# Performance work log

Measured on AMD Instinct MI355X. Metric: run time of the kernel, lower is better.

Reference implementation:

```python
import jax, jax.numpy as jnp
import numpy as np
import math

N_LEVELS = 4          # quadtree depth; leaves = 4**4 = 256
N_HEAD = 8
LN_EPS = 1e-5

def _tree_consts():
    # level d has 4**d nodes; offsets[d] = first node index of level d
    sizes = [4 ** d for d in range(N_LEVELS + 1)]
    offsets = np.concatenate([[0], np.cumsum(sizes)])
    n_nodes = int(offsets[-1])  # 341
    parent = np.full(n_nodes, -1, np.int64)
    for d in range(1, N_LEVELS + 1):
        idx = offsets[d] + np.arange(sizes[d])
        parent[idx] = offsets[d - 1] + np.arange(sizes[d]) // 4
    # chain[c, k] = k-th ancestor of c (k=0 -> self); padded by clamping at root
    chain = np.zeros((n_nodes, N_LEVELS + 1), np.int64)
    chain[:, 0] = np.arange(n_nodes)
    for k in range(1, N_LEVELS + 1):
        prev = chain[:, k - 1]
        chain[:, k] = np.where(parent[prev] >= 0, parent[prev], prev)
    nodes_at = [offsets[d] + np.arange(sizes[d]) for d in range(N_LEVELS + 1)]
    return chain, nodes_at, n_nodes

CHAIN, NODES_AT, N_NODES = _tree_consts()

def layernorm(x, g, b):
    m = jnp.mean(x, -1, keepdims=True)
    v = jnp.var(x, -1, keepdims=True)
    return (x - m) * jax.lax.rsqrt(v + LN_EPS) * g + b

def mhsa(x, w_qkv, b_qkv, w_proj, b_proj):
    B, N, E = x.shape
    hd = E // N_HEAD
    qkv = x @ w_qkv + b_qkv                       # (B, N, 3E)
    q, k, v = jnp.split(qkv, 3, axis=-1)
    sh = lambda t: t.reshape(B, N, N_HEAD, hd).transpose(0, 2, 1, 3)  # (B,H,N,hd)
    q, k, v = sh(q), sh(k), sh(v)
    att = jax.nn.softmax(jnp.einsum('bhqd,bhkd->bhqk', q, k) / math.sqrt(hd), axis=-1)
    o = jnp.einsum('bhqk,bhkd->bhqd', att, v).transpose(0, 2, 1, 3).reshape(B, N, E)
    return o @ w_proj + b_proj

def branch_mlp(x, M, b1, w2, b2):
    # Sparse equivalent of einsum('bni,bjmni->bmj', x, W1): W1[:, c, a, :]
    # is nonzero only for a in {c} U ancestors(c), with the weight matrix
    # depending only on (depth(c), depth(a)). Group nodes by depth and sum
    # over ancestor offsets k (depth(a) = d - k).
    B, N, E = x.shape
    h = jnp.zeros((B, N, 4 * E), x.dtype)
    for d in range(N_LEVELS + 1):
        nd = NODES_AT[d]                           # static numpy indices
        acc = jnp.zeros((B, nd.shape[0], 4 * E), x.dtype)
        for k in range(d + 1):
            src = CHAIN[nd, k]                     # ancestor at depth d-k
            acc = acc + jnp.einsum('bne,je->bnj', x[:, src, :], M[d, d - k])
        h = h.at[:, nd, :].set(acc)
    h = jax.nn.relu(h + b1[None, :, :])
    return h @ w2 + b2

def setup_inputs() -> dict:
    key = jax.random.key(0)
    ks = jax.random.split(key, 6)
    B, N, E = 64, N_NODES, 512
    s = 0.02
    return {
        'x': jax.random.normal(ks[0], (B, N, E), jnp.float32),
        'ln1_g': jnp.ones((E,), jnp.float32),
        'ln1_b': jnp.zeros((E,), jnp.float32),
        'w_qkv': jax.random.normal(ks[1], (E, 3 * E), jnp.float32) * s,
        'b_qkv': jnp.zeros((3 * E,), jnp.float32),
        'w_proj': jax.random.normal(ks[2], (E, E), jnp.float32) * s,
        'b_proj': jnp.zeros((E,), jnp.float32),
        'ln2_g': jnp.ones((E,), jnp.float32),
        'ln2_b': jnp.zeros((E,), jnp.float32),
        'mlp_M': jax.random.normal(ks[3], (N_LEVELS + 1, N_LEVELS + 1, 4 * E, E), jnp.float32) * s,
        'mlp_b1': jnp.zeros((N, 4 * E), jnp.float32),
        'w2': jax.random.normal(ks[4], (4 * E, E), jnp.float32) * s,
        'b2': jnp.zeros((E,), jnp.float32),
    }

def reference(x, ln1_g, ln1_b, w_qkv, b_qkv, w_proj, b_proj,
              ln2_g, ln2_b, mlp_M, mlp_b1, w2, b2):
    x = x + mhsa(layernorm(x, ln1_g, ln1_b), w_qkv, b_qkv, w_proj, b_proj)
    x = x + branch_mlp(layernorm(x, ln2_g, ln2_b), mlp_M, mlp_b1, w2, b2)
    return x
```

## Files before the change

### kernel.cpp

```cpp
#include <hip/hip_runtime.h>
#include <hip/hip_bf16.h>


typedef __attribute__((ext_vector_type(8))) __bf16 bf16x8;
typedef __attribute__((ext_vector_type(4))) float f32x4;
typedef __attribute__((ext_vector_type(4))) unsigned int u32x4;

#define GF_RELU    1
#define GF_OUTBF16 2

static __device__ __forceinline__ bf16x8 bzero8() {
    u32x4 z = {0u, 0u, 0u, 0u};
    return __builtin_bit_cast(bf16x8, z);
}

__global__ void transpose_bf16_kernel(const float* __restrict__ in,
                                      __hip_bfloat16* __restrict__ out,
                                      int K, int N, int log2K) {
    int idx = blockIdx.x * 256 + threadIdx.x;
    if (idx >= K * N) return;
    int n = idx >> log2K;
    int k = idx & (K - 1);
    out[idx] = __float2bfloat16(in[(size_t)k * N + n]);
}

__global__ void pack_wcat_kernel(const float* __restrict__ M,
                                 __hip_bfloat16* __restrict__ out) {
    int p = blockIdx.y;
    int s, d;
    if (p < 5)       { s = 0; d = p; }
    else if (p < 9)  { s = 1; d = p - 4; }
    else if (p < 12) { s = 2; d = p - 7; }
    else if (p < 14) { s = 3; d = p - 9; }
    else             { s = 4; d = 4; }
    const int base_lut[5] = {0, 5, 9, 12, 14};
    size_t idx = (size_t)blockIdx.x * 256 + threadIdx.x;
    const size_t MB = 2048ull * 512;
    out[(size_t)base_lut[s] * MB + (size_t)(d - s) * MB + idx] =
        __float2bfloat16(M[((size_t)d * 5 + s) * MB + idx]);
}

__global__ __launch_bounds__(256) void ln_kernel(const float* __restrict__ x,
                                                 const float* __restrict__ g,
                                                 const float* __restrict__ b,
                                                 __hip_bfloat16* __restrict__ out) {
    int tok = blockIdx.x;
    const float* xr = x + (size_t)tok * 512;
    int t = threadIdx.x;
    float v0 = xr[t], v1 = xr[t + 256];
    float s = v0 + v1;
    float s2 = v0 * v0 + v1 * v1;
    #pragma unroll
    for (int o = 32; o > 0; o >>= 1) {
        s  += __shfl_down(s, o);
        s2 += __shfl_down(s2, o);
    }
    __shared__ float ps[4], ps2[4];
    int w = t >> 6, lane = t & 63;
    if (lane == 0) { ps[w] = s; ps2[w] = s2; }
    __syncthreads();
    if (t == 0) {
        float ts = 0.f, ts2 = 0.f;
        #pragma unroll
        for (int i = 0; i < 4; i++) { ts += ps[i]; ts2 += ps2[i]; }
        ps[0] = ts * (1.f / 512.f);
        ps2[0] = ts2 * (1.f / 512.f);
    }
    __syncthreads();
    float m = ps[0];
    float var = ps2[0] - m * m;
    float r = rsqrtf(var + 1e-5f);
    out[(size_t)tok * 512 + t]       = __float2bfloat16((v0 - m) * r * g[t] + b[t]);
    out[(size_t)tok * 512 + t + 256] = __float2bfloat16((v1 - m) * r * g[t + 256] + b[t + 256]);
}

#define ATT_STR 72
__global__ __launch_bounds__(256) void attn_mfma_kernel(const __hip_bfloat16* __restrict__ qkv,
                                                        __hip_bfloat16* __restrict__ ctx) {
    __shared__ __bf16 kt_lds[64 * ATT_STR];
    __shared__ __bf16 vt_lds[64 * ATT_STR];
    __shared__ __bf16 pbuf[4 * 48 * ATT_STR];

    const int bh = blockIdx.x;
    const int half = blockIdx.y;
    const int b = bh >> 3, h = bh & 7;
    const int tid = threadIdx.x;
    const int w = tid >> 6, lane = tid & 63;
    const int q = lane >> 4, l16 = lane & 15;
    const int rowbase = half * 192 + w * 48;
    __bf16* pw = pbuf + w * 48 * ATT_STR;

    bf16x8 qf[3][2];
    #pragma unroll
    for (int mi = 0; mi < 3; mi++) {
        int row = rowbase + mi * 16 + l16;
        #pragma unroll
        for (int ks = 0; ks < 2; ks++) {
            if (row < 341)
                qf[mi][ks] = *(const bf16x8*)(qkv + (size_t)(b * 341 + row) * 1536 +
                                              h * 64 + ks * 32 + q * 8);
            else
                qf[mi][ks] = bzero8();
        }
    }

    f32x4 O[3][4];
    float mrun[3][4], lrun[3][4];
    #pragma unroll
    for (int mi = 0; mi < 3; mi++) {
        #pragma unroll
        for (int ni = 0; ni < 4; ni++) { f32x4 z = {0.f,0.f,0.f,0.f}; O[mi][ni] = z; }
        #pragma unroll
        for (int rr = 0; rr < 4; rr++) { mrun[mi][rr] = -1e30f; lrun[mi][rr] = 0.f; }
    }

    for (int kt6 = 0; kt6 < 6; kt6++) {
        const int kbase = kt6 * 64;
        __syncthreads();
        {
            int key = tid >> 2, kg = tid & 3;
            int gk = kbase + key;
            bf16x8 a0 = bzero8(), a1 = bzero8();
            if (gk < 341) {
                const __hip_bfloat16* src =
                    qkv + (size_t)(b * 341 + gk) * 1536 + 512 + h * 64 + kg * 16;
                a0 = *(const bf16x8*)src;
                a1 = *(const bf16x8*)(src + 8);
            }
            *(bf16x8*)(kt_lds + key * ATT_STR + kg * 16)     = a0;
            *(bf16x8*)(kt_lds + key * ATT_STR + kg * 16 + 8) = a1;
        }
        {
            int key = tid & 63, dg = tid >> 6;
            int gk = kbase + key;
            bf16x8 a0 = bzero8(), a1 = bzero8();
            if (gk < 341) {
                const __hip_bfloat16* src =
                    qkv + (size_t)(b * 341 + gk) * 1536 + 1024 + h * 64 + dg * 16;
                a0 = *(const bf16x8*)src;
                a1 = *(const bf16x8*)(src + 8);
            }
            #pragma unroll
            for (int j = 0; j < 8; j++) {
                vt_lds[(dg * 16 + j) * ATT_STR + key]     = a0[j];
                vt_lds[(dg * 16 + 8 + j) * ATT_STR + key] = a1[j];
            }
        }
        __syncthreads();

        f32x4 S[3][4];
        #pragma unroll
        for (int mi = 0; mi < 3; mi++)
            #pragma unroll
            for (int ni = 0; ni < 4; ni++) { f32x4 z = {0.f,0.f,0.f,0.f}; S[mi][ni] = z; }
        #pragma unroll
        for (int ks = 0; ks < 2; ks++) {
            bf16x8 bf_[4];
            #pragma unroll
            for (int ni = 0; ni < 4; ni++)
                bf_[ni] = *(const bf16x8*)(kt_lds + (ni * 16 + l16) * ATT_STR + ks * 32 + q * 8);
            #pragma unroll
            for (int mi = 0; mi < 3; mi++)
                #pragma unroll
                for (int ni = 0; ni < 4; ni++)
                    S[mi][ni] = __builtin_amdgcn_mfma_f32_16x16x32_bf16(qf[mi][ks], bf_[ni],
                                                                        S[mi][ni], 0, 0, 0);
        }

        float cmask[4];
        #pragma unroll
        for (int ni = 0; ni < 4; ni++)
            cmask[ni] = (kbase + ni * 16 + l16 < 341) ? 0.f : -1e30f;

        #pragma unroll
        for (int mi = 0; mi < 3; mi++) {
            #pragma unroll
            for (int rr = 0; rr < 4; rr++) {
                float rmax = -1e30f;
                #pragma unroll
                for (int ni = 0; ni < 4; ni++)
                    rmax = fmaxf(rmax, fmaf(S[mi][ni][rr], 0.125f, cmask[ni]));
                rmax = fmaxf(rmax, __shfl_xor(rmax, 1));
                rmax = fmaxf(rmax, __shfl_xor(rmax, 2));
                rmax = fmaxf(rmax, __shfl_xor(rmax, 4));
                rmax = fmaxf(rmax, __shfl_xor(rmax, 8));
                float mnew = fmaxf(mrun[mi][rr], rmax);
                float alpha = __expf(mrun[mi][rr] - mnew);
                mrun[mi][rr] = mnew;
                float psum = 0.f;
                #pragma unroll
                for (int ni = 0; ni < 4; ni++) {
                    float p = __expf(fmaf(S[mi][ni][rr], 0.125f, cmask[ni]) - mnew);
                    S[mi][ni][rr] = p;
                    psum += p;
                    O[mi][ni][rr] *= alpha;
                }
                psum += __shfl_xor(psum, 1);
                psum += __shfl_xor(psum, 2);
                psum += __shfl_xor(psum, 4);
                psum += __shfl_xor(psum, 8);
                lrun[mi][rr] = lrun[mi][rr] * alpha + psum;
            }
            #pragma unroll
            for (int ni = 0; ni < 4; ni++)
                #pragma unroll
                for (int rr = 0; rr < 4; rr++)
                    pw[(mi * 16 + q * 4 + rr) * ATT_STR + ni * 16 + l16] =
                        (__bf16)S[mi][ni][rr];
        }
        __syncthreads();

        #pragma unroll
        for (int ks = 0; ks < 2; ks++) {
            bf16x8 pf[3], vf[4];
            #pragma unroll
            for (int mi = 0; mi < 3; mi++)
                pf[mi] = *(const bf16x8*)(pw + (mi * 16 + l16) * ATT_STR + ks * 32 + q * 8);
            #pragma unroll
            for (int ni = 0; ni < 4; ni++)
                vf[ni] = *(const bf16x8*)(vt_lds + (ni * 16 + l16) * ATT_STR + ks * 32 + q * 8);
            #pragma unroll
            for (int mi = 0; mi < 3; mi++)
                #pragma unroll
                for (int ni = 0; ni < 4; ni++)
                    O[mi][ni] = __builtin_amdgcn_mfma_f32_16x16x32_bf16(pf[mi], vf[ni],
                                                                        O[mi][ni], 0, 0, 0);
        }
    }

    #pragma unroll
    for (int mi = 0; mi < 3; mi++) {
        #pragma unroll
        for (int rr = 0; rr < 4; rr++) {
            int row = rowbase + mi * 16 + q * 4 + rr;
            if (row >= 341) continue;
            float inv = 1.f / lrun[mi][rr];
            __hip_bfloat16* op = ctx + (size_t)(b * 341 + row) * 512 + h * 64;
            #pragma unroll
            for (int ni = 0; ni < 4; ni++)
                op[ni * 16 + l16] = __float2bfloat16(O[mi][ni][rr] * inv);
        }
    }
}

static __device__ __forceinline__ int xcd_remap(int bid, int nwg) {
    const int xcd = bid & 7, o = bid >> 3;
    const int qq = nwg >> 3, rr = nwg & 7;
    return (xcd < rr ? xcd * (qq + 1) : rr * (qq + 1) + (xcd - rr) * qq) + o;
}

template <bool GATHER>
static __device__ __forceinline__ void gemm128_body(
    __hip_bfloat16* As, __hip_bfloat16* Bs,
    const __hip_bfloat16* __restrict__ A, const __hip_bfloat16* __restrict__ Bt,
    const float* __restrict__ bias, const float* __restrict__ resid,
    float* __restrict__ Cf, __hip_bfloat16* __restrict__ Cb,
    int Mrows, int N, int K, int flags, int depth, int bm0, int bn0) {
    const int tid = threadIdx.x;
    const int r = tid >> 1;
    const int khalf = tid & 1;
    const int gr = bm0 + r;
    const int gn = bn0 + r;
    const int lane = tid & 63;
    const int w = tid >> 6;
    const int wm = (w >> 1) << 6;
    const int wn = (w & 1) << 6;
    const int q = lane >> 4;
    const int l16 = lane & 15;

    int wsl[4];
    #pragma unroll
    for (int j = 0; j < 4; j++)
        wsl[j] = ((((khalf << 2) | j) ^ (r & 7)) << 3);
    const int rs0 = ((q ^ (l16 & 7)) << 3);
    const int rs1 = (((4 + q) ^ (l16 & 7)) << 3);

    size_t abase;
    if (GATHER) {
        const int dsh = depth << 1;
        const int bmask = (1 << dsh) - 1;
        int b = gr >> dsh;
        int i = gr & bmask;
        int node = (0x55555555 & bmask) + i;
        abase = ((size_t)(b * 341 + node)) << 9;
    } else {
        abase = (size_t)gr * K;
    }

    f32x4 acc[4][4];
    #pragma unroll
    for (int i = 0; i < 4; i++)
        #pragma unroll
        for (int j = 0; j < 4; j++) {
            f32x4 z = {0.f, 0.f, 0.f, 0.f};
            acc[i][j] = z;
        }

    for (int k0 = 0; k0 < K; k0 += 64) {
        bf16x8 va[4], vb[4];
        if (gr < Mrows) {
            const bf16x8* p = (const bf16x8*)(A + abase + k0 + (khalf << 5));
            #pragma unroll
            for (int j = 0; j < 4; j++) va[j] = p[j];
        } else {
            #pragma unroll
            for (int j = 0; j < 4; j++) va[j] = bzero8();
        }
        {
            const bf16x8* p = (const bf16x8*)(Bt + (size_t)gn * K + k0 + (khalf << 5));
            #pragma unroll
            for (int j = 0; j < 4; j++) vb[j] = p[j];
        }
        __syncthreads();
        #pragma unroll
        for (int j = 0; j < 4; j++) {
            *(bf16x8*)(As + r * 64 + wsl[j]) = va[j];
            *(bf16x8*)(Bs + r * 64 + wsl[j]) = vb[j];
        }
        __syncthreads();
        bf16x8 af[4][2], bfr[4][2];
        #pragma unroll
        for (int mi = 0; mi < 4; mi++) {
            const __hip_bfloat16* rp = As + (wm + mi * 16 + l16) * 64;
            af[mi][0] = *(const bf16x8*)(rp + rs0);
            af[mi][1] = *(const bf16x8*)(rp + rs1);
        }
        #pragma unroll
        for (int ni = 0; ni < 4; ni++) {
            const __hip_bfloat16* rp = Bs + (wn + ni * 16 + l16) * 64;
            bfr[ni][0] = *(const bf16x8*)(rp + rs0);
            bfr[ni][1] = *(const bf16x8*)(rp + rs1);
        }
        #pragma unroll
        for (int ks = 0; ks < 2; ks++)
            #pragma unroll
            for (int mi = 0; mi < 4; mi++)
                #pragma unroll
                for (int ni = 0; ni < 4; ni++)
                    acc[mi][ni] = __builtin_amdgcn_mfma_f32_16x16x32_bf16(
                        af[mi][ks], bfr[ni][ks], acc[mi][ni], 0, 0, 0);
    }

    #pragma unroll
    for (int mi = 0; mi < 4; mi++) {
        #pragma unroll
        for (int rr = 0; rr < 4; rr++) {
            int grow = bm0 + wm + mi * 16 + q * 4 + rr;
            if (grow >= Mrows) continue;
            size_t obase = (size_t)grow * N;
            #pragma unroll
            for (int ni = 0; ni < 4; ni++) {
                int col = bn0 + wn + ni * 16 + l16;
                float v = acc[mi][ni][rr];
                if (bias) v += bias[col];
                if (resid) v += resid[obase + col];
                if (flags & GF_RELU) v = fmaxf(v, 0.f);
                if (flags & GF_OUTBF16)
                    Cb[obase + col] = __float2bfloat16(v);
                else
                    Cf[obase + col] = v;
            }
        }
    }
}

__global__ __launch_bounds__(256) void gemm128(
    const __hip_bfloat16* __restrict__ A, const __hip_bfloat16* __restrict__ Bt,
    const float* __restrict__ bias, const float* __restrict__ resid,
    float* __restrict__ Cf, __hip_bfloat16* __restrict__ Cb,
    int Mrows, int N, int K, int flags, int gridN) {
    __shared__ __hip_bfloat16 As[128 * 64];
    __shared__ __hip_bfloat16 Bs[128 * 64];
    const int lin = xcd_remap(blockIdx.x, gridDim.x);
    const int bx = lin / gridN;
    const int by = lin - bx * gridN;
    gemm128_body<false>(As, Bs, A, Bt, bias, resid, Cf, Cb,
                        Mrows, N, K, flags, 0, bx << 7, by << 7);
}

__global__ __launch_bounds__(256, 4) void gemm64(
    const __hip_bfloat16* __restrict__ A, const __hip_bfloat16* __restrict__ Bt,
    const float* __restrict__ bias, const float* __restrict__ resid,
    float* __restrict__ Cf, __hip_bfloat16* __restrict__ Cb,
    int Mrows, int N, int K, int flags, int gridN) {
    __shared__ __hip_bfloat16 As[64 * 64];
    __shared__ __hip_bfloat16 Bs[128 * 64];
    const int lin = xcd_remap(blockIdx.x, gridDim.x);
    const int bx = lin / gridN;
    const int by = lin - bx * gridN;
    const int bm0 = bx << 6, bn0 = by << 7;

    const int tid = threadIdx.x;
    const int ra = tid >> 2, kq = tid & 3;
    const int rb = tid >> 1, khalf = tid & 1;
    const int lane = tid & 63;
    const int w = tid >> 6;
    const int wn = w << 5;
    const int q = lane >> 4;
    const int l16 = lane & 15;

    const int gra = bm0 + ra;
    const int gnb = bn0 + rb;

    int wslA[2];
    #pragma unroll
    for (int j = 0; j < 2; j++)
        wslA[j] = ((((kq << 1) | j) ^ (ra & 7)) << 3);
    int wslB[4];
    #pragma unroll
    for (int j = 0; j < 4; j++)
        wslB[j] = ((((khalf << 2) | j) ^ (rb & 7)) << 3);
    const int rs0 = ((q ^ (l16 & 7)) << 3);
    const int rs1 = (((4 + q) ^ (l16 & 7)) << 3);

    const size_t abase = (size_t)gra * K;

    f32x4 acc[4][2];
    #pragma unroll
    for (int i = 0; i < 4; i++)
        #pragma unroll
        for (int j = 0; j < 2; j++) {
            f32x4 z = {0.f, 0.f, 0.f, 0.f};
            acc[i][j] = z;
        }

    for (int k0 = 0; k0 < K; k0 += 64) {
        bf16x8 va[2], vb[4];
        if (gra < Mrows) {
            const bf16x8* p = (const bf16x8*)(A + abase + k0 + (kq << 4));
            #pragma unroll
            for (int j = 0; j < 2; j++) va[j] = p[j];
        } else {
            #pragma unroll
            for (int j = 0; j < 2; j++) va[j] = bzero8();
        }
        {
            const bf16x8* p = (const bf16x8*)(Bt + (size_t)gnb * K + k0 + (khalf << 5));
            #pragma unroll
            for (int j = 0; j < 4; j++) vb[j] = p[j];
        }
        __syncthreads();
        #pragma unroll
        for (int j = 0; j < 2; j++)
            *(bf16x8*)(As + ra * 64 + wslA[j]) = va[j];
        #pragma unroll
        for (int j = 0; j < 4; j++)
            *(bf16x8*)(Bs + rb * 64 + wslB[j]) = vb[j];
        __syncthreads();
        bf16x8 af[4][2], bfr[2][2];
        #pragma unroll
        for (int mi = 0; mi < 4; mi++) {
            const __hip_bfloat16* rp = As + (mi * 16 + l16) * 64;
            af[mi][0] = *(const bf16x8*)(rp + rs0);
            af[mi][1] = *(const bf16x8*)(rp + rs1);
        }
        #pragma unroll
        for (int ni = 0; ni < 2; ni++) {
            const __hip_bfloat16* rp = Bs + (wn + ni * 16 + l16) * 64;
            bfr[ni][0] = *(const bf16x8*)(rp + rs0);
            bfr[ni][1] = *(const bf16x8*)(rp + rs1);
        }
        #pragma unroll
        for (int ks = 0; ks < 2; ks++)
            #pragma unroll
            for (int mi = 0; mi < 4; mi++)
                #pragma unroll
                for (int ni = 0; ni < 2; ni++)
                    acc[mi][ni] = __builtin_amdgcn_mfma_f32_16x16x32_bf16(
                        af[mi][ks], bfr[ni][ks], acc[mi][ni], 0, 0, 0);
    }

    #pragma unroll
    for (int mi = 0; mi < 4; mi++) {
        #pragma unroll
        for (int rr = 0; rr < 4; rr++) {
            int grow = bm0 + mi * 16 + q * 4 + rr;
            if (grow >= Mrows) continue;
            size_t obase = (size_t)grow * N;
            #pragma unroll
            for (int ni = 0; ni < 2; ni++) {
                int col = bn0 + wn + ni * 16 + l16;
                float v = acc[mi][ni][rr];
                if (bias) v += bias[col];
                if (resid) v += resid[obase + col];
                if (flags & GF_RELU) v = fmaxf(v, 0.f);
                if (flags & GF_OUTBF16)
                    Cb[obase + col] = __float2bfloat16(v);
                else
                    Cf[obase + col] = v;
            }
        }
    }
}

__global__ __launch_bounds__(256) void gemm_branch_fused(
    const __hip_bfloat16* __restrict__ xn, const __hip_bfloat16* __restrict__ wcat,
    __hip_bfloat16* __restrict__ Y) {
    __shared__ __hip_bfloat16 As[128 * 64];
    __shared__ __hip_bfloat16 Bs[128 * 64];
    const int lin = xcd_remap(blockIdx.x, gridDim.x);
    int s;
    if (lin < 80)        s = 0;
    else if (lin < 208)  s = 1;
    else if (lin < 592)  s = 2;
    else if (lin < 1616) s = 3;
    else                 s = 4;
    const int base_tab[5] = {0, 80, 208, 592, 1616};
    const int gn_tab[5]   = {80, 64, 48, 32, 16};
    const size_t yoff[5]  = {0, 655360, 2752512, 9043968, 25821184};
    const int wcat_off[5] = {0, 5, 9, 12, 14};
    const int loc = lin - base_tab[s];
    const int gn = gn_tab[s];
    const int bx = loc / gn;
    const int by = loc - bx * gn;
    const int Mrows = 64 << (s << 1);
    const int N = (5 - s) << 11;
    gemm128_body<true>(As, Bs, xn, wcat + (size_t)wcat_off[s] * (2048ull * 512),
                       nullptr, nullptr, nullptr, Y + yoff[s],
                       Mrows, N, 512, GF_OUTBF16, s, bx << 7, by << 7);
}

__global__ __launch_bounds__(256) void combine_kernel(const __hip_bfloat16* __restrict__ Y,
                                                      const float* __restrict__ b1,
                                                      __hip_bfloat16* __restrict__ h) {
    const size_t yoff[5] = {0, 655360, 2752512, 9043968, 25821184};
    int row = blockIdx.x;
    int b = row / 341;
    int node = row - b * 341;
    int d = (node >= 85) ? 4 : (node >= 21) ? 3 : (node >= 5) ? 2 : (node >= 1) ? 1 : 0;
    int i = node - (0x55555555 & ((1 << (d << 1)) - 1));
    int j = threadIdx.x << 3;

    float acc[8];
    const float* bp = b1 + (size_t)node * 2048 + j;
    f32x4 b0 = *(const f32x4*)bp;
    f32x4 b4 = *(const f32x4*)(bp + 4);
    #pragma unroll
    for (int u = 0; u < 4; u++) { acc[u] = b0[u]; acc[u + 4] = b4[u]; }

    #pragma unroll
    for (int s = 0; s < 5; s++) {
        if (s <= d) {
            int a = i >> ((d - s) << 1);
            int width = (5 - s) << 11;
            const bf16x8 v = *(const bf16x8*)(Y + yoff[s] +
                (size_t)((b << (s << 1)) + a) * width + ((d - s) << 11) + j);
            #pragma unroll
            for (int u = 0; u < 8; u++) acc[u] += (float)v[u];
        }
    }
    bf16x8 o;
    #pragma unroll
    for (int u = 0; u < 8; u++) o[u] = (__bf16)fmaxf(acc[u], 0.f);
    *(bf16x8*)(h + (size_t)row * 2048 + j) = o;
}

extern "C" void kernel_launch(void* const* d_in, const int* in_sizes, int n_in,
                              void* d_out, int out_size, void* d_ws, size_t ws_size,
                              hipStream_t stream) {
    const float* x      = (const float*)d_in[0];
    const float* ln1_g  = (const float*)d_in[1];
    const float* ln1_b  = (const float*)d_in[2];
    const float* w_qkv  = (const float*)d_in[3];
    const float* b_qkv  = (const float*)d_in[4];
    const float* w_proj = (const float*)d_in[5];
    const float* b_proj = (const float*)d_in[6];
    const float* ln2_g  = (const float*)d_in[7];
    const float* ln2_b  = (const float*)d_in[8];
    const float* mlp_M  = (const float*)d_in[9];
    const float* mlp_b1 = (const float*)d_in[10];
    const float* w2     = (const float*)d_in[11];
    const float* b2     = (const float*)d_in[12];
    float* out = (float*)d_out;

    const int M = 64 * 341;

    char* ws = (char*)d_ws;
    size_t off = 0;
    auto alloc = [&](size_t bytes) -> char* {
        char* p = ws + off;
        off += (bytes + 255) & ~(size_t)255;
        return p;
    };
    __hip_bfloat16* xn     = (__hip_bfloat16*)alloc((size_t)M * 512 * 2);
    __hip_bfloat16* wqkvT  = (__hip_bfloat16*)alloc(1536ull * 512 * 2);
    __hip_bfloat16* wprojT = (__hip_bfloat16*)alloc(512ull * 512 * 2);
    __hip_bfloat16* w2T    = (__hip_bfloat16*)alloc(512ull * 2048 * 2);
    __hip_bfloat16* wcat   = (__hip_bfloat16*)alloc(15ull * 2048 * 512 * 2);
    __hip_bfloat16* hbuf   = (__hip_bfloat16*)alloc((size_t)M * 2048 * 2);
    const size_t qkv_bytes = (size_t)M * 1536 * 2;
    const size_t y_bytes   = 59375616ull * 2;
    char* shared = alloc(y_bytes);
    __hip_bfloat16* qkv = (__hip_bfloat16*)shared;
    __hip_bfloat16* ctx = (__hip_bfloat16*)(shared + qkv_bytes);
    __hip_bfloat16* Y   = (__hip_bfloat16*)shared;
    if (off > ws_size) return;

    auto g128 = [&](const __hip_bfloat16* A, const __hip_bfloat16* Bt,
                    const float* bias, const float* resid, float* Cf,
                    __hip_bfloat16* Cb, int Mr, int N, int K, int flags) {
        int gm = (Mr + 127) >> 7, gn = N >> 7;
        gemm128<<<dim3(gm * gn), 256, 0, stream>>>(
            A, Bt, bias, resid, Cf, Cb, Mr, N, K, flags, gn);
    };
    auto g64 = [&](const __hip_bfloat16* A, const __hip_bfloat16* Bt,
                   const float* bias, const float* resid, float* Cf,
                   __hip_bfloat16* Cb, int Mr, int N, int K, int flags) {
        int gm = (Mr + 63) >> 6, gn = N >> 7;
        gemm64<<<dim3(gm * gn), 256, 0, stream>>>(
            A, Bt, bias, resid, Cf, Cb, Mr, N, K, flags, gn);
    };

    transpose_bf16_kernel<<<(512 * 1536 + 255) / 256, 256, 0, stream>>>(w_qkv, wqkvT, 512, 1536, 9);
    transpose_bf16_kernel<<<(512 * 512 + 255) / 256, 256, 0, stream>>>(w_proj, wprojT, 512, 512, 9);
    transpose_bf16_kernel<<<(2048 * 512 + 255) / 256, 256, 0, stream>>>(w2, w2T, 2048, 512, 11);
    pack_wcat_kernel<<<dim3(4096, 15), 256, 0, stream>>>(mlp_M, wcat);

    ln_kernel<<<M, 256, 0, stream>>>(x, ln1_g, ln1_b, xn);
    g128(xn, wqkvT, b_qkv, nullptr, nullptr, qkv, M, 1536, 512, GF_OUTBF16);
    attn_mfma_kernel<<<dim3(512, 2), 256, 0, stream>>>(qkv, ctx);
    g64(ctx, wprojT, b_proj, x, out, nullptr, M, 512, 512, 0);

    ln_kernel<<<M, 256, 0, stream>>>(out, ln2_g, ln2_b, xn);
    gemm_branch_fused<<<dim3(3664), 256, 0, stream>>>(xn, wcat, Y);
    combine_kernel<<<M, 256, 0, stream>>>(Y, mlp_b1, hbuf);
    g64(hbuf, w2T, b2, out, out, nullptr, M, 512, 2048, 0);
}
```

Baseline: 722.1 us.

## Split K across two wave groups in gemm64 with LDS reduction

```diff
diff --git a/kernel.cpp b/kernel.cpp
--- a/kernel.cpp
+++ b/kernel.cpp
@@ -378,42 +378,45 @@
                         Mrows, N, K, flags, 0, bx << 7, by << 7);
 }
 
-__global__ __launch_bounds__(256, 4) void gemm64(
+__global__ __launch_bounds__(512, 2) void gemm64k2(
     const __hip_bfloat16* __restrict__ A, const __hip_bfloat16* __restrict__ Bt,
     const float* __restrict__ bias, const float* __restrict__ resid,
     float* __restrict__ Cf, __hip_bfloat16* __restrict__ Cb,
     int Mrows, int N, int K, int flags, int gridN) {
-    __shared__ __hip_bfloat16 As[64 * 64];
-    __shared__ __hip_bfloat16 Bs[128 * 64];
+    __shared__ __align__(16) char smem_raw[49152];
+    __hip_bfloat16* As = (__hip_bfloat16*)smem_raw;
+    __hip_bfloat16* Bs = (__hip_bfloat16*)(smem_raw + 16384);
+    float* flds = (float*)smem_raw;
+
     const int lin = xcd_remap(blockIdx.x, gridDim.x);
     const int bx = lin / gridN;
     const int by = lin - bx * gridN;
     const int bm0 = bx << 6, bn0 = by << 7;
 
     const int tid = threadIdx.x;
-    const int ra = tid >> 2, kq = tid & 3;
-    const int rb = tid >> 1, khalf = tid & 1;
     const int lane = tid & 63;
     const int w = tid >> 6;
-    const int wn = w << 5;
+    const int kg = w >> 2;
+    const int wq = w & 3;
+    const int wn = wq << 5;
     const int q = lane >> 4;
     const int l16 = lane & 15;
 
+    const int ra = tid >> 3, ca = tid & 7;
+    const int rb = tid >> 2, cb = tid & 3;
     const int gra = bm0 + ra;
     const int gnb = bn0 + rb;
 
-    int wslA[2];
+    int wslA[2], wslB[4];
     #pragma unroll
     for (int j = 0; j < 2; j++)
-        wslA[j] = ((((kq << 1) | j) ^ (ra & 7)) << 3);
-    int wslB[4];
+        wslA[j] = ((((ca << 1) | j) ^ (ra & 7)) << 3);
     #pragma unroll
     for (int j = 0; j < 4; j++)
-        wslB[j] = ((((khalf << 2) | j) ^ (rb & 7)) << 3);
-    const int rs0 = ((q ^ (l16 & 7)) << 3);
-    const int rs1 = (((4 + q) ^ (l16 & 7)) << 3);
-
-    const size_t abase = (size_t)gra * K;
+        wslB[j] = ((((cb << 2) | j) ^ (rb & 7)) << 3);
+    int rs[2];
+    rs[0] = ((((kg << 3) | q)     ^ (l16 & 7)) << 3);
+    rs[1] = ((((kg << 3) | 4 | q) ^ (l16 & 7)) << 3);
 
     f32x4 acc[4][2];
     #pragma unroll
@@ -424,10 +427,10 @@
             acc[i][j] = z;
         }
 
-    for (int k0 = 0; k0 < K; k0 += 64) {
+    for (int k0 = 0; k0 < K; k0 += 128) {
         bf16x8 va[2], vb[4];
         if (gra < Mrows) {
-            const bf16x8* p = (const bf16x8*)(A + abase + k0 + (kq << 4));
+            const bf16x8* p = (const bf16x8*)(A + (size_t)gra * K + k0 + (ca << 4));
             #pragma unroll
             for (int j = 0; j < 2; j++) va[j] = p[j];
         } else {
@@ -435,30 +438,30 @@
             for (int j = 0; j < 2; j++) va[j] = bzero8();
         }
         {
-            const bf16x8* p = (const bf16x8*)(Bt + (size_t)gnb * K + k0 + (khalf << 5));
+            const bf16x8* p = (const bf16x8*)(Bt + (size_t)gnb * K + k0 + (cb << 5));
             #pragma unroll
             for (int j = 0; j < 4; j++) vb[j] = p[j];
         }
         __syncthreads();
         #pragma unroll
         for (int j = 0; j < 2; j++)
-            *(bf16x8*)(As + ra * 64 + wslA[j]) = va[j];
+            *(bf16x8*)(As + ra * 128 + wslA[j]) = va[j];
         #pragma unroll
         for (int j = 0; j < 4; j++)
-            *(bf16x8*)(Bs + rb * 64 + wslB[j]) = vb[j];
+            *(bf16x8*)(Bs + rb * 128 + wslB[j]) = vb[j];
         __syncthreads();
         bf16x8 af[4][2], bfr[2][2];
         #pragma unroll
         for (int mi = 0; mi < 4; mi++) {
-            const __hip_bfloat16* rp = As + (mi * 16 + l16) * 64;
-            af[mi][0] = *(const bf16x8*)(rp + rs0);
-            af[mi][1] = *(const bf16x8*)(rp + rs1);
+            const __hip_bfloat16* rp = As + (mi * 16 + l16) * 128;
+            af[mi][0] = *(const bf16x8*)(rp + rs[0]);
+            af[mi][1] = *(const bf16x8*)(rp + rs[1]);
         }
         #pragma unroll
         for (int ni = 0; ni < 2; ni++) {
-            const __hip_bfloat16* rp = Bs + (wn + ni * 16 + l16) * 64;
-            bfr[ni][0] = *(const bf16x8*)(rp + rs0);
-            bfr[ni][1] = *(const bf16x8*)(rp + rs1);
+            const __hip_bfloat16* rp = Bs + (wn + ni * 16 + l16) * 128;
+            bfr[ni][0] = *(const bf16x8*)(rp + rs[0]);
+            bfr[ni][1] = *(const bf16x8*)(rp + rs[1]);
         }
         #pragma unroll
         for (int ks = 0; ks < 2; ks++)
@@ -470,24 +473,45 @@
                         af[mi][ks], bfr[ni][ks], acc[mi][ni], 0, 0, 0);
     }
 
-    #pragma unroll
-    for (int mi = 0; mi < 4; mi++) {
-        #pragma unroll
-        for (int rr = 0; rr < 4; rr++) {
-            int grow = bm0 + mi * 16 + q * 4 + rr;
-            if (grow >= Mrows) continue;
-            size_t obase = (size_t)grow * N;
+    __syncthreads();
+    const int FSTRIDE = 36;
+    if (kg == 1) {
+        float* fp = flds + (tid - 256) * FSTRIDE;
+        #pragma unroll
+        for (int mi = 0; mi < 4; mi++)
+            #pragma unroll
+            for (int ni = 0; ni < 2; ni++)
+                *(f32x4*)(fp + (mi * 2 + ni) * 4) = acc[mi][ni];
+    }
+    __syncthreads();
+    if (kg == 0) {
+        const float* fp = flds + tid * FSTRIDE;
+        #pragma unroll
+        for (int mi = 0; mi < 4; mi++)
             #pragma unroll
             for (int ni = 0; ni < 2; ni++) {
-                int col = bn0 + wn + ni * 16 + l16;
-                float v = acc[mi][ni][rr];
-                if (bias) v += bias[col];
-                if (resid) v += resid[obase + col];
-                if (flags & GF_RELU) v = fmaxf(v, 0.f);
-                if (flags & GF_OUTBF16)
-                    Cb[obase + col] = __float2bfloat16(v);
-                else
-                    Cf[obase + col] = v;
+                f32x4 v = *(const f32x4*)(fp + (mi * 2 + ni) * 4);
+                acc[mi][ni] += v;
+            }
+        #pragma unroll
+        for (int mi = 0; mi < 4; mi++) {
+            #pragma unroll
+            for (int rr = 0; rr < 4; rr++) {
+                int grow = bm0 + mi * 16 + q * 4 + rr;
+                if (grow >= Mrows) continue;
+                size_t obase = (size_t)grow * N;
+                #pragma unroll
+                for (int ni = 0; ni < 2; ni++) {
+                    int col = bn0 + wn + ni * 16 + l16;
+                    float v = acc[mi][ni][rr];
+                    if (bias) v += bias[col];
+                    if (resid) v += resid[obase + col];
+                    if (flags & GF_RELU) v = fmaxf(v, 0.f);
+                    if (flags & GF_OUTBF16)
+                        Cb[obase + col] = __float2bfloat16(v);
+                    else
+                        Cf[obase + col] = v;
+                }
             }
         }
     }
@@ -607,7 +631,7 @@
                    const float* bias, const float* resid, float* Cf,
                    __hip_bfloat16* Cb, int Mr, int N, int K, int flags) {
         int gm = (Mr + 63) >> 6, gn = N >> 7;
-        gemm64<<<dim3(gm * gn), 256, 0, stream>>>(
+        gemm64k2<<<dim3(gm * gn), 512, 0, stream>>>(
             A, Bt, bias, resid, Cf, Cb, Mr, N, K, flags, gn);
     };
 
```

Measured after the change: 765.4 us. 1.06x slower.
